# Kernel tuning notes

Hardware: AMD Instinct MI355X
Metric: run time of the kernel (lower is better)

## Reference

```python
import jax, jax.numpy as jnp
import numpy as np

K = 5            # carafe kernel size
CK = 3           # content conv kernel size = max(3, K-2)
EMB = 64         # embedding size
FILTERS = 128    # output filters


def conv1x1(x, w, b=None):
    y = jnp.einsum('bhwc,co->bhwo', x, w)
    return y if b is None else y + b


def conv_same(x, w, b):
    y = jax.lax.conv_general_dilated(x, w, (1, 1), 'SAME',
                                     dimension_numbers=('NHWC', 'HWIO', 'NHWC'))
    return y + b


def up2(x):
    return jnp.repeat(jnp.repeat(x, 2, axis=1), 2, axis=2)


def setup_inputs() -> dict:
    key = jax.random.key(0)
    ks = jax.random.split(key, 12)
    B, H, W, Cf = 2, 128, 128, 128
    h, w, Cc = 64, 64, 128
    s = 0.05
    return {
        'fine': jax.random.normal(ks[0], (B, H, W, Cf), jnp.float32),
        'coarse': jax.random.normal(ks[1], (B, h, w, Cc), jnp.float32),
        # gate 1x1 conv (Cc -> 1)
        'w_gate': jax.random.normal(ks[2], (Cc, 1), jnp.float32) * s,
        'b_gate': jnp.zeros((1,), jnp.float32),
        # SemiShift: fine 1x1 (no bias), coarse 1x1 (bias), shared content conv (EMB -> K*K)
        'w_sfine': jax.random.normal(ks[3], (Cf, EMB), jnp.float32) * s,
        'w_scoarse': jax.random.normal(ks[4], (Cc, EMB), jnp.float32) * s,
        'b_scoarse': jnp.zeros((EMB,), jnp.float32),
        'w_content': jax.random.normal(ks[5], (CK, CK, EMB, K * K), jnp.float32) * s,
        'b_content': jnp.zeros((K * K,), jnp.float32),
        # output 1x1 convs
        'w_coarse': jax.random.normal(ks[6], (Cc, FILTERS), jnp.float32) * s,
        'b_coarse': jnp.zeros((FILTERS,), jnp.float32),
        'w_fineout': jax.random.normal(ks[7], (FILTERS, FILTERS), jnp.float32) * s,
        'b_fineout': jnp.zeros((FILTERS,), jnp.float32),
    }


def reference(fine, coarse, w_gate, b_gate, w_sfine, w_scoarse, b_scoarse,
              w_content, b_content, w_coarse, b_coarse, w_fineout, b_fineout):
    B, h, w, Cc = coarse.shape
    H, W = fine.shape[1], fine.shape[2]

    # gate branch
    gate = jax.nn.sigmoid(conv1x1(coarse, w_gate, b_gate))
    gate = up2(gate)  # [B,H,W,1]

    # SemiShift kernel prediction
    f = conv1x1(fine, w_sfine)                     # no bias
    f = conv_same(f, w_content, b_content)         # [B,H,W,K*K]
    c = conv1x1(coarse, w_scoarse, b_scoarse)
    c = conv_same(c, w_content, b_content)         # [B,h,w,K*K]
    kernel = jax.nn.softmax(f + up2(c), axis=-1)   # [B,H,W,K*K]

    # CarafeConvolution: extract_patches (TF layout: [pos, ch] innermost) + NN up + grouped matmul
    p = K // 2
    xp = jnp.pad(coarse, ((0, 0), (p, p), (p, p), (0, 0)))
    patches = jnp.stack([xp[:, r:r + h, cc:cc + w, :]
                         for r in range(K) for cc in range(K)], axis=3)  # [B,h,w,K*K,Cc]
    patches = patches.reshape(B, h, w, K * K * Cc)
    patches = up2(patches)                          # [B,H,W,K*K*Cc]
    # faithful reshape as in source (group_size=1): (B,H,W,Cc,K*K)
    feat = patches.reshape(B, H, W, Cc, K * K)
    carafe = jnp.einsum('bhwck,bhwk->bhwc', feat, kernel)  # [B,H,W,Cc]

    coarse_out = conv1x1(carafe, w_coarse, b_coarse)        # [B,H,W,FILTERS]
    fine_out = conv1x1(coarse_out, w_fineout, b_fineout)    # note: applied to coarse_out as in source
    return gate * fine_out + (1.0 - gate) * coarse_out
```

## Files before the change

kernel.cpp:

```cpp
#include <hip/hip_runtime.h>
#include <hip/hip_bf16.h>
#include <cstdint>
#include <cstddef>

#define KSZ 5
#define KK 25
#define EMB 64
#define CC 128
#define FILTERS 128

typedef __attribute__((ext_vector_type(8))) short short8;
typedef __attribute__((ext_vector_type(4))) float floatx4;

__device__ inline unsigned short f32_to_bf16(float f) {
    union { float f; unsigned u; } v; v.f = f;
    unsigned u = v.u;
    unsigned r = u + 0x7FFF + ((u >> 16) & 1);
    return (unsigned short)(r >> 16);
}

#define XS_P 136
__global__ __launch_bounds__(256) void embed_both_kernel(
        const float* __restrict__ xf, const float* __restrict__ wsf,
        const float* __restrict__ xc, const float* __restrict__ wsc,
        const float* __restrict__ bias_c,
        unsigned short* __restrict__ yf, unsigned short* __restrict__ yc,
        int nf, int nemb,
        const float* __restrict__ w_content, const float* __restrict__ w_coarse,
        const float* __restrict__ w_fineout,
        unsigned short* __restrict__ wconT, unsigned short* __restrict__ wcT,
        unsigned short* __restrict__ wfT) {
    int tid = threadIdx.x;

    if ((int)blockIdx.x >= nemb) {
        int idx = (blockIdx.x - nemb) * 256 + tid;
        if (idx < 18432) {
            int n = idx / 576, k = idx - n * 576;
            float v = (n < 25) ? w_content[k * 25 + n] : 0.0f;
            wconT[idx] = f32_to_bf16(v);
        } else if (idx < 34816) {
            int j = idx - 18432;
            int o = j >> 7, k = j & 127;
            wcT[j] = f32_to_bf16(w_coarse[k * 128 + o]);
        } else {
            int j = idx - 34816;
            int o = j >> 7, k = j & 127;
            wfT[j] = f32_to_bf16(w_fineout[k * 128 + o]);
        }
        return;
    }

    __shared__ unsigned short Xs[128 * XS_P];
    __shared__ unsigned short Ws[64 * XS_P];
    bool is_f = (int)blockIdx.x < nf;
    int blk = is_f ? blockIdx.x : (blockIdx.x - nf);
    const float* x = is_f ? xf : xc;
    const float* wsrcf = is_f ? wsf : wsc;
    const float* bias = is_f ? nullptr : bias_c;
    unsigned short* y = is_f ? yf : yc;
    size_t row0 = (size_t)blk * 128;

    {
        const float4* src = (const float4*)(x + row0 * 128);
        for (int ci = tid; ci < 4096; ci += 256) {
            int r = ci >> 5, c4 = ci & 31;
            float4 v = src[ci];
            uint2 u;
            u.x = (unsigned)f32_to_bf16(v.x) | ((unsigned)f32_to_bf16(v.y) << 16);
            u.y = (unsigned)f32_to_bf16(v.z) | ((unsigned)f32_to_bf16(v.w) << 16);
            *(uint2*)(&Xs[r * XS_P + c4 * 4]) = u;
        }
        for (int ci = tid; ci < 2048; ci += 256) {
            int k = ci >> 4;
            int n4 = (ci & 15) * 4;
            float4 v = *(const float4*)(wsrcf + k * 64 + n4);
            Ws[(n4 + 0) * XS_P + k] = f32_to_bf16(v.x);
            Ws[(n4 + 1) * XS_P + k] = f32_to_bf16(v.y);
            Ws[(n4 + 2) * XS_P + k] = f32_to_bf16(v.z);
            Ws[(n4 + 3) * XS_P + k] = f32_to_bf16(v.w);
        }
    }
    __syncthreads();

    int wid = tid >> 6, lane = tid & 63;
    int lr = lane & 15, hi = lane >> 4, lk = hi * 8;

    floatx4 acc[2][4];
    #pragma unroll
    for (int mi = 0; mi < 2; ++mi)
        #pragma unroll
        for (int ni = 0; ni < 4; ++ni)
            acc[mi][ni] = (floatx4){0.f, 0.f, 0.f, 0.f};

    #pragma unroll
    for (int kk = 0; kk < 128; kk += 32) {
        short8 a[2], bb[4];
        #pragma unroll
        for (int mi = 0; mi < 2; ++mi)
            a[mi] = *(const short8*)(&Xs[(wid * 32 + mi * 16 + lr) * XS_P + kk + lk]);
        #pragma unroll
        for (int ni = 0; ni < 4; ++ni)
            bb[ni] = *(const short8*)(&Ws[(ni * 16 + lr) * XS_P + kk + lk]);
        #pragma unroll
        for (int mi = 0; mi < 2; ++mi)
            #pragma unroll
            for (int ni = 0; ni < 4; ++ni)
                acc[mi][ni] = __builtin_amdgcn_mfma_f32_16x16x32_bf16(a[mi], bb[ni], acc[mi][ni], 0, 0, 0);
    }

    #pragma unroll
    for (int mi = 0; mi < 2; ++mi) {
        #pragma unroll
        for (int ni = 0; ni < 4; ++ni) {
            int col = ni * 16 + lr;
            float bs = bias ? bias[col] : 0.0f;
            #pragma unroll
            for (int j = 0; j < 4; ++j) {
                int row = wid * 32 + mi * 16 + hi * 4 + j;
                y[(row0 + row) * EMB + col] = f32_to_bf16(acc[mi][ni][j] + bs);
            }
        }
    }
}

#define SP 72
#define SB 584
__global__ __launch_bounds__(256) void content_both_kernel(
        const unsigned short* __restrict__ embf,
        const unsigned short* __restrict__ embc,
        const unsigned short* __restrict__ wT,
        const float* __restrict__ bias,
        float* __restrict__ yf, float* __restrict__ yc,
        int nf) {
    __shared__ unsigned short Es[6 * 34 * SP];
    __shared__ unsigned short Bs[32 * SB];
    int tid = threadIdx.x;
    bool is_f = (int)blockIdx.x < nf;
    int blk = is_f ? blockIdx.x : (blockIdx.x - nf);
    const unsigned short* emb = is_f ? embf : embc;
    float* y = is_f ? yf : yc;
    int HT = is_f ? 32 : 16;
    int WT = is_f ? 4 : 2;
    int Hh = is_f ? 128 : 64;
    int Ww = is_f ? 128 : 64;

    int bx = blk % WT;
    int t = blk / WT;
    int by = t % HT;
    int b = t / HT;

    for (int ci = tid; ci < 1632; ci += 256) {
        int pi = ci >> 3, e8 = ci & 7;
        int hy = pi / 34, hx = pi - hy * 34;
        int gy = by * 4 + hy - 1, gx = bx * 32 + hx - 1;
        uint4 v = {0u, 0u, 0u, 0u};
        if (gy >= 0 && gy < Hh && gx >= 0 && gx < Ww)
            v = *(const uint4*)(emb + (((size_t)(b * Hh + gy)) * Ww + gx) * EMB + e8 * 8);
        *(uint4*)(&Es[pi * SP + e8 * 8]) = v;
    }
    for (int ci = tid; ci < 2304; ci += 256) {
        int n = ci / 72, k8 = ci - n * 72;
        *(uint4*)(&Bs[n * SB + k8 * 8]) = *(const uint4*)(wT + n * 576 + k8 * 8);
    }
    __syncthreads();

    int wid = tid >> 6, lane = tid & 63;
    int lr = lane & 15, hi = lane >> 4, lk = hi * 8;

    floatx4 acc[2][2];
    #pragma unroll
    for (int mi = 0; mi < 2; ++mi)
        #pragma unroll
        for (int ni = 0; ni < 2; ++ni)
            acc[mi][ni] = (floatx4){0.f, 0.f, 0.f, 0.f};

    #pragma unroll
    for (int tap = 0; tap < 9; ++tap) {
        int dy = tap / 3, dx = tap - dy * 3;
        #pragma unroll
        for (int ks = 0; ks < 2; ++ks) {
            short8 a[2], bb[2];
            #pragma unroll
            for (int mi = 0; mi < 2; ++mi) {
                int p = wid * 32 + mi * 16 + lr;
                int r = p >> 5, c = p & 31;
                a[mi] = *(const short8*)(&Es[((r + dy) * 34 + (c + dx)) * SP + ks * 32 + lk]);
            }
            #pragma unroll
            for (int ni = 0; ni < 2; ++ni)
                bb[ni] = *(const short8*)(&Bs[(ni * 16 + lr) * SB + tap * 64 + ks * 32 + lk]);
            #pragma unroll
            for (int mi = 0; mi < 2; ++mi)
                #pragma unroll
                for (int ni = 0; ni < 2; ++ni)
                    acc[mi][ni] = __builtin_amdgcn_mfma_f32_16x16x32_bf16(a[mi], bb[ni], acc[mi][ni], 0, 0, 0);
        }
    }

    #pragma unroll
    for (int mi = 0; mi < 2; ++mi) {
        #pragma unroll
        for (int ni = 0; ni < 2; ++ni) {
            int n = ni * 16 + lr;
            if (n < KK) {
                float bs = bias[n];
                #pragma unroll
                for (int j = 0; j < 4; ++j) {
                    int p = wid * 32 + mi * 16 + hi * 4 + j;
                    int r = p >> 5, c = p & 31;
                    size_t gq = ((size_t)(b * Hh + by * 4 + r)) * Ww + bx * 32 + c;
                    y[gq * KK + n] = acc[mi][ni][j] + bs;
                }
            }
        }
    }
}

#define LDSP 136
__global__ __launch_bounds__(256) void carafe_final_kernel(
        const float* __restrict__ coarse,
        const float* __restrict__ f_conv,
        const float* __restrict__ c_conv,
        const float* __restrict__ w_gate,
        const float* __restrict__ b_gate,
        const unsigned short* __restrict__ WcT,
        const unsigned short* __restrict__ WfT,
        const float* __restrict__ b_coarse,
        const float* __restrict__ b_fineout,
        float* __restrict__ out) {
    __shared__ __align__(16) char smem[58624];
    float* patches = (float*)smem;
    float* wsm     = (float*)(smem + 32768);
    float* g_lds   = (float*)(smem + 40960);
    unsigned short* Ws = (unsigned short*)smem;
    unsigned short* Xs = (unsigned short*)(smem + 41216);

    const int h = 64, w = 64, H2 = 128, W2 = 128;
    int tid = threadIdx.x;
    int blk = blockIdx.x;
    int cx0 = (blk & 15) * 4;
    int cy0 = ((blk >> 4) & 15) * 4;
    int b = blk >> 8;

    for (int ci = tid; ci < 2048; ci += 256) {
        int pi = ci >> 5;
        int c4 = (ci & 31) << 2;
        int sy = cy0 - 2 + (pi >> 3);
        int sx = cx0 - 2 + (pi & 7);
        float4 v = {0.f, 0.f, 0.f, 0.f};
        if (sy >= 0 && sy < h && sx >= 0 && sx < w)
            v = *(const float4*)(coarse + (((size_t)(b * h + sy)) * w + sx) * CC + c4);
        *(float4*)(&patches[pi * 128 + c4]) = v;
    }

    int wid = tid >> 6, lane = tid & 63;
    {
        int k = lane & 31;
        #pragma unroll
        for (int pass = 0; pass < 8; ++pass) {
            int fp = wid * 16 + pass * 2 + (lane >> 5);
            int fry = fp >> 3, frx = fp & 7;
            int fy = 2 * cy0 + fry, fx = 2 * cx0 + frx;
            int cy = cy0 + (fry >> 1), cx = cx0 + (frx >> 1);
            size_t fq = ((size_t)(b * H2 + fy)) * W2 + fx;
            size_t cq = ((size_t)(b * h + cy)) * w + cx;
            float v = -1e30f;
            if (k < KK)
                v = f_conv[fq * KK + k] + c_conv[cq * KK + k];
            float m = v;
            #pragma unroll
            for (int mask = 16; mask > 0; mask >>= 1)
                m = fmaxf(m, __shfl_xor(m, mask, 32));
            float e = (k < KK) ? __expf(v - m) : 0.0f;
            float s = e;
            #pragma unroll
            for (int mask = 16; mask > 0; mask >>= 1)
                s += __shfl_xor(s, mask, 32);
            wsm[fp * 32 + k] = e / s;
        }
    }
    __syncthreads();

    {
        int cp = tid >> 4;
        int part = tid & 15;
        int pidx = ((cp >> 2) + 2) * 8 + (cp & 3) + 2;
        const float* pc = patches + pidx * 128 + part * 8;
        float4 a0 = *(const float4*)(pc);
        float4 a1 = *(const float4*)(pc + 4);
        float4 g0 = *(const float4*)(w_gate + part * 8);
        float4 g1 = *(const float4*)(w_gate + part * 8 + 4);
        float acc = a0.x * g0.x + a0.y * g0.y + a0.z * g0.z + a0.w * g0.w
                  + a1.x * g1.x + a1.y * g1.y + a1.z * g1.z + a1.w * g1.w;
        #pragma unroll
        for (int mask = 8; mask > 0; mask >>= 1)
            acc += __shfl_xor(acc, mask, 16);
        if (part == 0) {
            float z = acc + b_gate[0];
            g_lds[cp] = 1.0f / (1.0f + __expf(-z));
        }
    }

    {
        int ph = tid >> 7;
        int c  = tid & 127;
        int offs[KK];
        int c25 = c * 25;
        #pragma unroll
        for (int j = 0; j < KK; ++j) {
            int i = c25 + j;
            int p = i >> 7;
            int ch = i & 127;
            int pd = (p * 205) >> 10;
            int pm = p - pd * 5;
            offs[j] = (pd * 8 + pm) * 128 + ch;
        }
        for (int cp = 0; cp < 16; ++cp) {
            int ry = cp >> 2, rx = cp & 3;
            int cpbase = (ry * 8 + rx) * 128;
            int fpA = (2 * ry + ph) * 8 + 2 * rx;
            float w0[28], w1[28];
            #pragma unroll
            for (int j4 = 0; j4 < 7; ++j4) {
                *(float4*)(&w0[j4 * 4]) = *(const float4*)(&wsm[fpA * 32 + j4 * 4]);
                *(float4*)(&w1[j4 * 4]) = *(const float4*)(&wsm[(fpA + 1) * 32 + j4 * 4]);
            }
            float acc0 = 0.0f, acc1 = 0.0f;
            #pragma unroll
            for (int j = 0; j < KK; ++j) {
                float pv = patches[cpbase + offs[j]];
                acc0 += w0[j] * pv;
                acc1 += w1[j] * pv;
            }
            Xs[fpA * LDSP + c] = f32_to_bf16(acc0);
            Xs[(fpA + 1) * LDSP + c] = f32_to_bf16(acc1);
        }
    }
    __syncthreads();

    {
        const uint4* wsrc = (const uint4*)WcT;
        for (int ci = tid; ci < 2048; ci += 256) {
            int r = ci >> 4, c = ci & 15;
            *(uint4*)(&Ws[r * LDSP + c * 8]) = wsrc[ci];
        }
    }
    __syncthreads();

    int wm = wid >> 1, wn = wid & 1;
    int lr = lane & 15;
    int lk = (lane >> 4) * 8;
    int lrow4 = (lane >> 4) * 4;

    floatx4 acc1[2][4];
    #pragma unroll
    for (int mi = 0; mi < 2; ++mi)
        #pragma unroll
        for (int ni = 0; ni < 4; ++ni)
            acc1[mi][ni] = (floatx4){0.f, 0.f, 0.f, 0.f};

    #pragma unroll
    for (int kk = 0; kk < 128; kk += 32) {
        short8 a[2], bb[4];
        #pragma unroll
        for (int mi = 0; mi < 2; ++mi)
            a[mi] = *(const short8*)(&Xs[(wm * 32 + mi * 16 + lr) * LDSP + kk + lk]);
        #pragma unroll
        for (int ni = 0; ni < 4; ++ni)
            bb[ni] = *(const short8*)(&Ws[(wn * 64 + ni * 16 + lr) * LDSP + kk + lk]);
        #pragma unroll
        for (int mi = 0; mi < 2; ++mi)
            #pragma unroll
            for (int ni = 0; ni < 4; ++ni)
                acc1[mi][ni] = __builtin_amdgcn_mfma_f32_16x16x32_bf16(a[mi], bb[ni], acc1[mi][ni], 0, 0, 0);
    }
    __syncthreads();

    {
        const uint4* wsrc = (const uint4*)WfT;
        for (int ci = tid; ci < 2048; ci += 256) {
            int r = ci >> 4, c = ci & 15;
            *(uint4*)(&Ws[r * LDSP + c * 8]) = wsrc[ci];
        }
    }
    #pragma unroll
    for (int mi = 0; mi < 2; ++mi) {
        #pragma unroll
        for (int ni = 0; ni < 4; ++ni) {
            int col = wn * 64 + ni * 16 + lr;
            float bc = b_coarse[col];
            #pragma unroll
            for (int j = 0; j < 4; ++j) {
                int row = wm * 32 + mi * 16 + lrow4 + j;
                float v = acc1[mi][ni][j] + bc;
                acc1[mi][ni][j] = v;
                Xs[row * LDSP + col] = f32_to_bf16(v);
            }
        }
    }
    __syncthreads();

    floatx4 acc2[2][4];
    #pragma unroll
    for (int mi = 0; mi < 2; ++mi)
        #pragma unroll
        for (int ni = 0; ni < 4; ++ni)
            acc2[mi][ni] = (floatx4){0.f, 0.f, 0.f, 0.f};

    #pragma unroll
    for (int kk = 0; kk < 128; kk += 32) {
        short8 a[2], bb[4];
        #pragma unroll
        for (int mi = 0; mi < 2; ++mi)
            a[mi] = *(const short8*)(&Xs[(wm * 32 + mi * 16 + lr) * LDSP + kk + lk]);
        #pragma unroll
        for (int ni = 0; ni < 4; ++ni)
            bb[ni] = *(const short8*)(&Ws[(wn * 64 + ni * 16 + lr) * LDSP + kk + lk]);
        #pragma unroll
        for (int mi = 0; mi < 2; ++mi)
            #pragma unroll
            for (int ni = 0; ni < 4; ++ni)
                acc2[mi][ni] = __builtin_amdgcn_mfma_f32_16x16x32_bf16(a[mi], bb[ni], acc2[mi][ni], 0, 0, 0);
    }

    #pragma unroll
    for (int mi = 0; mi < 2; ++mi) {
        #pragma unroll
        for (int ni = 0; ni < 4; ++ni) {
            int col = wn * 64 + ni * 16 + lr;
            float bf = b_fineout[col];
            #pragma unroll
            for (int j = 0; j < 4; ++j) {
                int row = wm * 32 + mi * 16 + lrow4 + j;
                int fry = row >> 3, frx = row & 7;
                float g = g_lds[((fry >> 1) << 2) + (frx >> 1)];
                int fy = 2 * cy0 + fry, fx = 2 * cx0 + frx;
                size_t q = ((size_t)(b * H2 + fy)) * W2 + fx;
                float co = acc1[mi][ni][j];
                float fo = acc2[mi][ni][j] + bf;
                out[q * FILTERS + col] = g * fo + (1.0f - g) * co;
            }
        }
    }
}

extern "C" void kernel_launch(void* const* d_in, const int* in_sizes, int n_in,
                              void* d_out, int out_size, void* d_ws, size_t ws_size,
                              hipStream_t stream) {
    const float* fine      = (const float*)d_in[0];
    const float* coarse    = (const float*)d_in[1];
    const float* w_gate    = (const float*)d_in[2];
    const float* b_gate    = (const float*)d_in[3];
    const float* w_sfine   = (const float*)d_in[4];
    const float* w_scoarse = (const float*)d_in[5];
    const float* b_scoarse = (const float*)d_in[6];
    const float* w_content = (const float*)d_in[7];
    const float* b_content = (const float*)d_in[8];
    const float* w_coarse  = (const float*)d_in[9];
    const float* b_coarse  = (const float*)d_in[10];
    const float* w_fineout = (const float*)d_in[11];
    const float* b_fineout = (const float*)d_in[12];
    float* out = (float*)d_out;

    const int B = 2, H = 128, W = 128, h = 64, w = 64;
    const int MF = B * H * W;
    const int MC = B * h * w;

    char* ws = (char*)d_ws;
    size_t off = 0;
    auto alloc = [&](size_t bytes) {
        void* p = ws + off;
        off = (off + bytes + 255) & ~(size_t)255;
        return p;
    };
    unsigned short* f_emb    = (unsigned short*)alloc((size_t)MF * EMB * 2);
    unsigned short* c_emb    = (unsigned short*)alloc((size_t)MC * EMB * 2);
    float* f_conv            = (float*)alloc((size_t)MF * KK * 4);
    float* c_conv            = (float*)alloc((size_t)MC * KK * 4);
    unsigned short* wconT    = (unsigned short*)alloc(32 * 576 * 2);
    unsigned short* wcT      = (unsigned short*)alloc(128 * 128 * 2);
    unsigned short* wfT      = (unsigned short*)alloc(128 * 128 * 2);

    const int NEF = MF / 128;
    const int NEC = MC / 128;
    const int NEB = NEF + NEC;
    const int NWT = 200;
    const int NCF = B * (H / 4) * (W / 32);
    const int NCC = B * (h / 4) * (w / 32);

    embed_both_kernel<<<NEB + NWT, 256, 0, stream>>>(fine, w_sfine, coarse, w_scoarse, b_scoarse,
                                                     f_emb, c_emb, NEF, NEB,
                                                     w_content, w_coarse, w_fineout,
                                                     wconT, wcT, wfT);
    content_both_kernel<<<NCF + NCC, 256, 0, stream>>>(f_emb, c_emb, wconT, b_content,
                                                       f_conv, c_conv, NCF);
    carafe_final_kernel<<<B * 16 * 16, 256, 0, stream>>>(coarse, f_conv, c_conv, w_gate, b_gate,
                                                         wcT, wfT, b_coarse, b_fineout, out);
}
```

Before: 49.96 us.

## Fuse embedding 1x1 conv into content 3x3 conv kernel with halo recompute

Merges the embedding GEMM and the 3x3 content convolution into one kernel. Each tile now computes the bf16 embeddings for its 6x34 halo region directly from fp32 inputs into shared memory, so the intermediate embedding tensor no longer makes a round trip through global memory and one launch is removed. The price is recomputing halo pixels (about 1.6x the embedding work), transposing the content weights per block with a scalar loop, and using more shared memory per block, which may lower occupancy.

```diff
diff --git a/kernel.cpp b/kernel.cpp
--- a/kernel.cpp
+++ b/kernel.cpp
@@ -19,125 +19,44 @@
     return (unsigned short)(r >> 16);
 }
 
+#define SP 72
+#define SB 584
 #define XS_P 136
-__global__ __launch_bounds__(256) void embed_both_kernel(
+#define WS_OFF 29376
+__global__ __launch_bounds__(256) void embcont_kernel(
         const float* __restrict__ xf, const float* __restrict__ wsf,
         const float* __restrict__ xc, const float* __restrict__ wsc,
         const float* __restrict__ bias_c,
-        unsigned short* __restrict__ yf, unsigned short* __restrict__ yc,
-        int nf, int nemb,
-        const float* __restrict__ w_content, const float* __restrict__ w_coarse,
-        const float* __restrict__ w_fineout,
-        unsigned short* __restrict__ wconT, unsigned short* __restrict__ wcT,
-        unsigned short* __restrict__ wfT) {
+        const float* __restrict__ w_content,
+        const float* __restrict__ bias_con,
+        float* __restrict__ yf, float* __restrict__ yc,
+        int nf, int ncont,
+        const float* __restrict__ w_coarse, const float* __restrict__ w_fineout,
+        unsigned short* __restrict__ wcT, unsigned short* __restrict__ wfT) {
     int tid = threadIdx.x;
 
-    if ((int)blockIdx.x >= nemb) {
-        int idx = (blockIdx.x - nemb) * 256 + tid;
-        if (idx < 18432) {
-            int n = idx / 576, k = idx - n * 576;
-            float v = (n < 25) ? w_content[k * 25 + n] : 0.0f;
-            wconT[idx] = f32_to_bf16(v);
-        } else if (idx < 34816) {
-            int j = idx - 18432;
-            int o = j >> 7, k = j & 127;
-            wcT[j] = f32_to_bf16(w_coarse[k * 128 + o]);
+    if ((int)blockIdx.x >= ncont) {
+        int idx = (blockIdx.x - ncont) * 256 + tid;
+        if (idx < 16384) {
+            int o = idx >> 7, k = idx & 127;
+            wcT[idx] = f32_to_bf16(w_coarse[k * 128 + o]);
         } else {
-            int j = idx - 34816;
+            int j = idx - 16384;
             int o = j >> 7, k = j & 127;
             wfT[j] = f32_to_bf16(w_fineout[k * 128 + o]);
         }
         return;
     }
 
-    __shared__ unsigned short Xs[128 * XS_P];
-    __shared__ unsigned short Ws[64 * XS_P];
+    __shared__ __align__(16) char smem[66752];
+    unsigned short* Es = (unsigned short*)smem;
+    unsigned short* Ws = (unsigned short*)(smem + WS_OFF);
+    unsigned short* Bs = (unsigned short*)(smem + WS_OFF);
+
     bool is_f = (int)blockIdx.x < nf;
     int blk = is_f ? blockIdx.x : (blockIdx.x - nf);
     const float* x = is_f ? xf : xc;
-    const float* wsrcf = is_f ? wsf : wsc;
-    const float* bias = is_f ? nullptr : bias_c;
-    unsigned short* y = is_f ? yf : yc;
-    size_t row0 = (size_t)blk * 128;
-
-    {
-        const float4* src = (const float4*)(x + row0 * 128);
-        for (int ci = tid; ci < 4096; ci += 256) {
-            int r = ci >> 5, c4 = ci & 31;
-            float4 v = src[ci];
-            uint2 u;
-            u.x = (unsigned)f32_to_bf16(v.x) | ((unsigned)f32_to_bf16(v.y) << 16);
-            u.y = (unsigned)f32_to_bf16(v.z) | ((unsigned)f32_to_bf16(v.w) << 16);
-            *(uint2*)(&Xs[r * XS_P + c4 * 4]) = u;
-        }
-        for (int ci = tid; ci < 2048; ci += 256) {
-            int k = ci >> 4;
-            int n4 = (ci & 15) * 4;
-            float4 v = *(const float4*)(wsrcf + k * 64 + n4);
-            Ws[(n4 + 0) * XS_P + k] = f32_to_bf16(v.x);
-            Ws[(n4 + 1) * XS_P + k] = f32_to_bf16(v.y);
-            Ws[(n4 + 2) * XS_P + k] = f32_to_bf16(v.z);
-            Ws[(n4 + 3) * XS_P + k] = f32_to_bf16(v.w);
-        }
-    }
-    __syncthreads();
-
-    int wid = tid >> 6, lane = tid & 63;
-    int lr = lane & 15, hi = lane >> 4, lk = hi * 8;
-
-    floatx4 acc[2][4];
-    #pragma unroll
-    for (int mi = 0; mi < 2; ++mi)
-        #pragma unroll
-        for (int ni = 0; ni < 4; ++ni)
-            acc[mi][ni] = (floatx4){0.f, 0.f, 0.f, 0.f};
-
-    #pragma unroll
-    for (int kk = 0; kk < 128; kk += 32) {
-        short8 a[2], bb[4];
-        #pragma unroll
-        for (int mi = 0; mi < 2; ++mi)
-            a[mi] = *(const short8*)(&Xs[(wid * 32 + mi * 16 + lr) * XS_P + kk + lk]);
-        #pragma unroll
-        for (int ni = 0; ni < 4; ++ni)
-            bb[ni] = *(const short8*)(&Ws[(ni * 16 + lr) * XS_P + kk + lk]);
-        #pragma unroll
-        for (int mi = 0; mi < 2; ++mi)
-            #pragma unroll
-            for (int ni = 0; ni < 4; ++ni)
-                acc[mi][ni] = __builtin_amdgcn_mfma_f32_16x16x32_bf16(a[mi], bb[ni], acc[mi][ni], 0, 0, 0);
-    }
-
-    #pragma unroll
-    for (int mi = 0; mi < 2; ++mi) {
-        #pragma unroll
-        for (int ni = 0; ni < 4; ++ni) {
-            int col = ni * 16 + lr;
-            float bs = bias ? bias[col] : 0.0f;
-            #pragma unroll
-            for (int j = 0; j < 4; ++j) {
-                int row = wid * 32 + mi * 16 + hi * 4 + j;
-                y[(row0 + row) * EMB + col] = f32_to_bf16(acc[mi][ni][j] + bs);
-            }
-        }
-    }
-}
-
-#define SP 72
-#define SB 584
-__global__ __launch_bounds__(256) void content_both_kernel(
-        const unsigned short* __restrict__ embf,
-        const unsigned short* __restrict__ embc,
-        const unsigned short* __restrict__ wT,
-        const float* __restrict__ bias,
-        float* __restrict__ yf, float* __restrict__ yc,
-        int nf) {
-    __shared__ unsigned short Es[6 * 34 * SP];
-    __shared__ unsigned short Bs[32 * SB];
-    int tid = threadIdx.x;
-    bool is_f = (int)blockIdx.x < nf;
-    int blk = is_f ? blockIdx.x : (blockIdx.x - nf);
-    const unsigned short* emb = is_f ? embf : embc;
+    const float* wemb = is_f ? wsf : wsc;
     float* y = is_f ? yf : yc;
     int HT = is_f ? 32 : 16;
     int WT = is_f ? 4 : 2;
@@ -149,23 +68,85 @@
     int by = t % HT;
     int b = t / HT;
 
-    for (int ci = tid; ci < 1632; ci += 256) {
-        int pi = ci >> 3, e8 = ci & 7;
-        int hy = pi / 34, hx = pi - hy * 34;
-        int gy = by * 4 + hy - 1, gx = bx * 32 + hx - 1;
-        uint4 v = {0u, 0u, 0u, 0u};
-        if (gy >= 0 && gy < Hh && gx >= 0 && gx < Ww)
-            v = *(const uint4*)(emb + (((size_t)(b * Hh + gy)) * Ww + gx) * EMB + e8 * 8);
-        *(uint4*)(&Es[pi * SP + e8 * 8]) = v;
-    }
-    for (int ci = tid; ci < 2304; ci += 256) {
-        int n = ci / 72, k8 = ci - n * 72;
-        *(uint4*)(&Bs[n * SB + k8 * 8]) = *(const uint4*)(wT + n * 576 + k8 * 8);
+    for (int ci = tid; ci < 2048; ci += 256) {
+        int k = ci >> 4;
+        int n4 = (ci & 15) * 4;
+        float4 v = *(const float4*)(wemb + k * 64 + n4);
+        Ws[(n4 + 0) * XS_P + k] = f32_to_bf16(v.x);
+        Ws[(n4 + 1) * XS_P + k] = f32_to_bf16(v.y);
+        Ws[(n4 + 2) * XS_P + k] = f32_to_bf16(v.z);
+        Ws[(n4 + 3) * XS_P + k] = f32_to_bf16(v.w);
     }
     __syncthreads();
 
     int wid = tid >> 6, lane = tid & 63;
     int lr = lane & 15, hi = lane >> 4, lk = hi * 8;
+
+    {
+        int nfr = (wid == 0) ? 4 : 3;
+        int rbase = (wid == 0) ? 0 : 64 + (wid - 1) * 48;
+        for (int f = 0; f < nfr; ++f) {
+            int frag0 = rbase + f * 16;
+            int px = frag0 + lr;
+            int hy = px / 34, hx = px - hy * 34;
+            int gy = by * 4 + hy - 1, gx = bx * 32 + hx - 1;
+            bool valid = (px < 204) && ((unsigned)gy < (unsigned)Hh) && ((unsigned)gx < (unsigned)Ww);
+            const float* xr = x + (((size_t)(b * Hh + gy)) * Ww + gx) * 128;
+
+            floatx4 accE[4];
+            #pragma unroll
+            for (int ni = 0; ni < 4; ++ni)
+                accE[ni] = (floatx4){0.f, 0.f, 0.f, 0.f};
+
+            #pragma unroll
+            for (int kk = 0; kk < 4; ++kk) {
+                float4 a0 = {0.f, 0.f, 0.f, 0.f}, a1 = {0.f, 0.f, 0.f, 0.f};
+                if (valid) {
+                    a0 = *(const float4*)(xr + kk * 32 + lk);
+                    a1 = *(const float4*)(xr + kk * 32 + lk + 4);
+                }
+                unsigned short ah[8];
+                ah[0] = f32_to_bf16(a0.x); ah[1] = f32_to_bf16(a0.y);
+                ah[2] = f32_to_bf16(a0.z); ah[3] = f32_to_bf16(a0.w);
+                ah[4] = f32_to_bf16(a1.x); ah[5] = f32_to_bf16(a1.y);
+                ah[6] = f32_to_bf16(a1.z); ah[7] = f32_to_bf16(a1.w);
+                short8 a = *(const short8*)ah;
+                #pragma unroll
+                for (int ni = 0; ni < 4; ++ni) {
+                    short8 bb = *(const short8*)(&Ws[(ni * 16 + lr) * XS_P + kk * 32 + lk]);
+                    accE[ni] = __builtin_amdgcn_mfma_f32_16x16x32_bf16(a, bb, accE[ni], 0, 0, 0);
+                }
+            }
+            #pragma unroll
+            for (int ni = 0; ni < 4; ++ni) {
+                int col = ni * 16 + lr;
+                float bs = is_f ? 0.0f : bias_c[col];
+                #pragma unroll
+                for (int j = 0; j < 4; ++j) {
+                    int pw = frag0 + hi * 4 + j;
+                    if (pw < 204) {
+                        int hyw = pw / 34, hxw = pw - hyw * 34;
+                        int gyw = by * 4 + hyw - 1, gxw = bx * 32 + hxw - 1;
+                        bool vw = ((unsigned)gyw < (unsigned)Hh) && ((unsigned)gxw < (unsigned)Ww);
+                        Es[pw * SP + col] = vw ? f32_to_bf16(accE[ni][j] + bs) : (unsigned short)0;
+                    }
+                }
+            }
+        }
+    }
+    __syncthreads();
+
+    {
+        int n = tid >> 3;
+        int koff = (tid & 7) * 72;
+        bool live = (n < KK);
+        for (int kk = 0; kk < 72; ++kk) {
+            int k = koff + kk;
+            float v = live ? w_content[k * 25 + n] : 0.0f;
+            Bs[n * SB + k] = f32_to_bf16(v);
+        }
+    }
+    __syncthreads();
 
     floatx4 acc[2][2];
     #pragma unroll
@@ -203,7 +184,7 @@
         for (int ni = 0; ni < 2; ++ni) {
             int n = ni * 16 + lr;
             if (n < KK) {
-                float bs = bias[n];
+                float bs = bias_con[n];
                 #pragma unroll
                 for (int j = 0; j < 4; ++j) {
                     int p = wid * 32 + mi * 16 + hi * 4 + j;
@@ -473,27 +454,20 @@
         off = (off + bytes + 255) & ~(size_t)255;
         return p;
     };
-    unsigned short* f_emb    = (unsigned short*)alloc((size_t)MF * EMB * 2);
-    unsigned short* c_emb    = (unsigned short*)alloc((size_t)MC * EMB * 2);
     float* f_conv            = (float*)alloc((size_t)MF * KK * 4);
     float* c_conv            = (float*)alloc((size_t)MC * KK * 4);
-    unsigned short* wconT    = (unsigned short*)alloc(32 * 576 * 2);
     unsigned short* wcT      = (unsigned short*)alloc(128 * 128 * 2);
     unsigned short* wfT      = (unsigned short*)alloc(128 * 128 * 2);
 
-    const int NEF = MF / 128;
-    const int NEC = MC / 128;
-    const int NEB = NEF + NEC;
-    const int NWT = 200;
     const int NCF = B * (H / 4) * (W / 32);
     const int NCC = B * (h / 4) * (w / 32);
-
-    embed_both_kernel<<<NEB + NWT, 256, 0, stream>>>(fine, w_sfine, coarse, w_scoarse, b_scoarse,
-                                                     f_emb, c_emb, NEF, NEB,
-                                                     w_content, w_coarse, w_fineout,
-                                                     wconT, wcT, wfT);
-    content_both_kernel<<<NCF + NCC, 256, 0, stream>>>(f_emb, c_emb, wconT, b_content,
-                                                       f_conv, c_conv, NCF);
+    const int NCONT = NCF + NCC;
+    const int NWT = 128;
+
+    embcont_kernel<<<NCONT + NWT, 256, 0, stream>>>(fine, w_sfine, coarse, w_scoarse, b_scoarse,
+                                                    w_content, b_content,
+                                                    f_conv, c_conv, NCF, NCONT,
+                                                    w_coarse, w_fineout, wcT, wfT);
     carafe_final_kernel<<<B * 16 * 16, 256, 0, stream>>>(coarse, f_conv, c_conv, w_gate, b_gate,
                                                          wcT, wfT, b_coarse, b_fineout, out);
 }
```

After: 69.21 us. 38.5% more time.

## Load embed A-operand directly from global and reuse patches across four fine pixels

Applied to the files above, without the earlier changes.

The embedding GEMM kernel no longer stages the activation tile in shared memory. Each wave loads its fp32 rows straight from global memory, converts them to bf16 in registers and feeds the MFMA, and the block tile shrinks from 128 to 64 rows, doubling the grid. In the carafe kernel each thread now handles 8 coarse pixels and writes all four upsampled fine pixels from one patch gather, where before it handled 16 coarse pixels for half the fine pixels. The aim is to cut LDS traffic, shared-memory footprint and the number of patch reads, at the cost of more registers per thread and less coalesced global loads in the embed kernel.

```diff
diff --git a/kernel.cpp b/kernel.cpp
--- a/kernel.cpp
+++ b/kernel.cpp
@@ -50,7 +50,6 @@
         return;
     }
 
-    __shared__ unsigned short Xs[128 * XS_P];
     __shared__ unsigned short Ws[64 * XS_P];
     bool is_f = (int)blockIdx.x < nf;
     int blk = is_f ? blockIdx.x : (blockIdx.x - nf);
@@ -58,67 +57,55 @@
     const float* wsrcf = is_f ? wsf : wsc;
     const float* bias = is_f ? nullptr : bias_c;
     unsigned short* y = is_f ? yf : yc;
-    size_t row0 = (size_t)blk * 128;
-
-    {
-        const float4* src = (const float4*)(x + row0 * 128);
-        for (int ci = tid; ci < 4096; ci += 256) {
-            int r = ci >> 5, c4 = ci & 31;
-            float4 v = src[ci];
-            uint2 u;
-            u.x = (unsigned)f32_to_bf16(v.x) | ((unsigned)f32_to_bf16(v.y) << 16);
-            u.y = (unsigned)f32_to_bf16(v.z) | ((unsigned)f32_to_bf16(v.w) << 16);
-            *(uint2*)(&Xs[r * XS_P + c4 * 4]) = u;
-        }
-        for (int ci = tid; ci < 2048; ci += 256) {
-            int k = ci >> 4;
-            int n4 = (ci & 15) * 4;
-            float4 v = *(const float4*)(wsrcf + k * 64 + n4);
-            Ws[(n4 + 0) * XS_P + k] = f32_to_bf16(v.x);
-            Ws[(n4 + 1) * XS_P + k] = f32_to_bf16(v.y);
-            Ws[(n4 + 2) * XS_P + k] = f32_to_bf16(v.z);
-            Ws[(n4 + 3) * XS_P + k] = f32_to_bf16(v.w);
-        }
+    size_t row0 = (size_t)blk * 64;
+
+    for (int ci = tid; ci < 2048; ci += 256) {
+        int k = ci >> 4;
+        int n4 = (ci & 15) * 4;
+        float4 v = *(const float4*)(wsrcf + k * 64 + n4);
+        Ws[(n4 + 0) * XS_P + k] = f32_to_bf16(v.x);
+        Ws[(n4 + 1) * XS_P + k] = f32_to_bf16(v.y);
+        Ws[(n4 + 2) * XS_P + k] = f32_to_bf16(v.z);
+        Ws[(n4 + 3) * XS_P + k] = f32_to_bf16(v.w);
     }
     __syncthreads();
 
     int wid = tid >> 6, lane = tid & 63;
     int lr = lane & 15, hi = lane >> 4, lk = hi * 8;
 
-    floatx4 acc[2][4];
-    #pragma unroll
-    for (int mi = 0; mi < 2; ++mi)
-        #pragma unroll
-        for (int ni = 0; ni < 4; ++ni)
-            acc[mi][ni] = (floatx4){0.f, 0.f, 0.f, 0.f};
-
-    #pragma unroll
-    for (int kk = 0; kk < 128; kk += 32) {
-        short8 a[2], bb[4];
-        #pragma unroll
-        for (int mi = 0; mi < 2; ++mi)
-            a[mi] = *(const short8*)(&Xs[(wid * 32 + mi * 16 + lr) * XS_P + kk + lk]);
-        #pragma unroll
-        for (int ni = 0; ni < 4; ++ni)
-            bb[ni] = *(const short8*)(&Ws[(ni * 16 + lr) * XS_P + kk + lk]);
-        #pragma unroll
-        for (int mi = 0; mi < 2; ++mi)
-            #pragma unroll
-            for (int ni = 0; ni < 4; ++ni)
-                acc[mi][ni] = __builtin_amdgcn_mfma_f32_16x16x32_bf16(a[mi], bb[ni], acc[mi][ni], 0, 0, 0);
-    }
-
-    #pragma unroll
-    for (int mi = 0; mi < 2; ++mi) {
+    int arow = wid * 16 + lr;
+    const float* xr = x + (row0 + arow) * 128;
+
+    floatx4 acc[4];
+    #pragma unroll
+    for (int ni = 0; ni < 4; ++ni)
+        acc[ni] = (floatx4){0.f, 0.f, 0.f, 0.f};
+
+    #pragma unroll
+    for (int kk = 0; kk < 4; ++kk) {
+        float4 a0 = *(const float4*)(xr + kk * 32 + lk);
+        float4 a1 = *(const float4*)(xr + kk * 32 + lk + 4);
+        unsigned short ah[8];
+        ah[0] = f32_to_bf16(a0.x); ah[1] = f32_to_bf16(a0.y);
+        ah[2] = f32_to_bf16(a0.z); ah[3] = f32_to_bf16(a0.w);
+        ah[4] = f32_to_bf16(a1.x); ah[5] = f32_to_bf16(a1.y);
+        ah[6] = f32_to_bf16(a1.z); ah[7] = f32_to_bf16(a1.w);
+        short8 a = *(const short8*)ah;
         #pragma unroll
         for (int ni = 0; ni < 4; ++ni) {
-            int col = ni * 16 + lr;
-            float bs = bias ? bias[col] : 0.0f;
-            #pragma unroll
-            for (int j = 0; j < 4; ++j) {
-                int row = wid * 32 + mi * 16 + hi * 4 + j;
-                y[(row0 + row) * EMB + col] = f32_to_bf16(acc[mi][ni][j] + bs);
-            }
+            short8 bb = *(const short8*)(&Ws[(ni * 16 + lr) * XS_P + kk * 32 + lk]);
+            acc[ni] = __builtin_amdgcn_mfma_f32_16x16x32_bf16(a, bb, acc[ni], 0, 0, 0);
+        }
+    }
+
+    #pragma unroll
+    for (int ni = 0; ni < 4; ++ni) {
+        int col = ni * 16 + lr;
+        float bs = bias ? bias[col] : 0.0f;
+        #pragma unroll
+        for (int j = 0; j < 4; ++j) {
+            int row = wid * 16 + hi * 4 + j;
+            y[(row0 + row) * EMB + col] = f32_to_bf16(acc[ni][j] + bs);
         }
     }
 }
@@ -302,12 +289,12 @@
     }
 
     {
-        int ph = tid >> 7;
-        int c  = tid & 127;
-        int offs[KK];
+        int c   = tid & 127;
+        int cpg = tid >> 7;
+        int offs[28];
         int c25 = c * 25;
         #pragma unroll
-        for (int j = 0; j < KK; ++j) {
+        for (int j = 0; j < 28; ++j) {
             int i = c25 + j;
             int p = i >> 7;
             int ch = i & 127;
@@ -315,25 +302,36 @@
             int pm = p - pd * 5;
             offs[j] = (pd * 8 + pm) * 128 + ch;
         }
-        for (int cp = 0; cp < 16; ++cp) {
+        #pragma unroll
+        for (int it = 0; it < 8; ++it) {
+            int cp = cpg * 8 + it;
             int ry = cp >> 2, rx = cp & 3;
             int cpbase = (ry * 8 + rx) * 128;
-            int fpA = (2 * ry + ph) * 8 + 2 * rx;
-            float w0[28], w1[28];
+            int fpA = (2 * ry) * 8 + 2 * rx;
+            float a00 = 0.f, a01 = 0.f, a10 = 0.f, a11 = 0.f;
             #pragma unroll
             for (int j4 = 0; j4 < 7; ++j4) {
-                *(float4*)(&w0[j4 * 4]) = *(const float4*)(&wsm[fpA * 32 + j4 * 4]);
-                *(float4*)(&w1[j4 * 4]) = *(const float4*)(&wsm[(fpA + 1) * 32 + j4 * 4]);
+                float4 wA = *(const float4*)(&wsm[fpA * 32 + j4 * 4]);
+                float4 wB = *(const float4*)(&wsm[(fpA + 1) * 32 + j4 * 4]);
+                float4 wC = *(const float4*)(&wsm[(fpA + 8) * 32 + j4 * 4]);
+                float4 wD = *(const float4*)(&wsm[(fpA + 9) * 32 + j4 * 4]);
+                #pragma unroll
+                for (int jj = 0; jj < 4; ++jj) {
+                    float pv = patches[cpbase + offs[j4 * 4 + jj]];
+                    float wa = (jj == 0) ? wA.x : (jj == 1) ? wA.y : (jj == 2) ? wA.z : wA.w;
+                    float wb = (jj == 0) ? wB.x : (jj == 1) ? wB.y : (jj == 2) ? wB.z : wB.w;
+                    float wc = (jj == 0) ? wC.x : (jj == 1) ? wC.y : (jj == 2) ? wC.z : wC.w;
+                    float wd = (jj == 0) ? wD.x : (jj == 1) ? wD.y : (jj == 2) ? wD.z : wD.w;
+                    a00 += wa * pv;
+                    a01 += wb * pv;
+                    a10 += wc * pv;
+                    a11 += wd * pv;
+                }
             }
-            float acc0 = 0.0f, acc1 = 0.0f;
-            #pragma unroll
-            for (int j = 0; j < KK; ++j) {
-                float pv = patches[cpbase + offs[j]];
-                acc0 += w0[j] * pv;
-                acc1 += w1[j] * pv;
-            }
-            Xs[fpA * LDSP + c] = f32_to_bf16(acc0);
-            Xs[(fpA + 1) * LDSP + c] = f32_to_bf16(acc1);
+            Xs[fpA * LDSP + c]       = f32_to_bf16(a00);
+            Xs[(fpA + 1) * LDSP + c] = f32_to_bf16(a01);
+            Xs[(fpA + 8) * LDSP + c] = f32_to_bf16(a10);
+            Xs[(fpA + 9) * LDSP + c] = f32_to_bf16(a11);
         }
     }
     __syncthreads();
@@ -481,8 +479,8 @@
     unsigned short* wcT      = (unsigned short*)alloc(128 * 128 * 2);
     unsigned short* wfT      = (unsigned short*)alloc(128 * 128 * 2);
 
-    const int NEF = MF / 128;
-    const int NEC = MC / 128;
+    const int NEF = MF / 64;
+    const int NEC = MC / 64;
     const int NEB = NEF + NEC;
     const int NWT = 200;
     const int NCF = B * (H / 4) * (W / 32);
```

Result: faster. 47.41 us (-5.1%).
